# Kernel optimization log

Hardware: AMD Instinct MI355X
Metric: run time of the kernel (lower is better)

Reference implementation:

```python
import jax, jax.numpy as jnp
import numpy as np

NUM_TOKENS = 8192
CODEBOOK_DIM = 64
ENC_CH = 512
DEC_CH = 512
B, H, W = 16, 32, 32


def setup_inputs() -> dict:
    key = jax.random.key(0)
    ks = jax.random.split(key, 6)
    return {
        "x": jax.random.normal(ks[0], (B, ENC_CH, H, W), dtype=jnp.float32),
        "w_in": jax.random.normal(ks[1], (CODEBOOK_DIM, ENC_CH), dtype=jnp.float32) * 0.05,
        "b_in": jax.random.normal(ks[2], (CODEBOOK_DIM,), dtype=jnp.float32) * 0.05,
        "embedding": jax.random.normal(ks[3], (NUM_TOKENS, CODEBOOK_DIM), dtype=jnp.float32),
        "w_out": jax.random.normal(ks[4], (DEC_CH, CODEBOOK_DIM), dtype=jnp.float32) * 0.05,
        "b_out": jax.random.normal(ks[5], (DEC_CH,), dtype=jnp.float32) * 0.05,
    }


def reference(x, w_in, b_in, embedding, w_out, b_out):
    # encoder projection: 1x1 conv == channel matmul. x: [B,C,H,W] -> [B,d,H,W]
    z = jnp.einsum('bchw,dc->bdhw', x, w_in) + b_in[None, :, None, None]

    # VectorQuantizer.forward -----------------------------------------
    # permute to channels-last and flatten: [B,H,W,d] -> [N,d]
    inputs = jnp.transpose(z, (0, 2, 3, 1))  # [B,H,W,d]
    flat = inputs.reshape(-1, CODEBOOK_DIM)  # [N,d]

    # squared L2 distances to every codebook entry: [N,K]
    distances = (jnp.sum(flat ** 2, axis=1, keepdims=True)
                 + jnp.sum(embedding ** 2, axis=1)[None, :]
                 - 2.0 * flat @ embedding.T)
    indices = jnp.argmin(distances, axis=1)  # [N] int

    # one-hot @ embedding in the original == direct gather
    quantized = jnp.take(embedding, indices, axis=0).reshape(inputs.shape)

    # straight-through estimator
    quantized = inputs + jax.lax.stop_gradient(quantized - inputs)
    tokens = jnp.transpose(quantized, (0, 3, 1, 2))  # [B,d,H,W]

    # decoder projection: 1x1 conv
    projected = jnp.einsum('bdhw,od->bohw', tokens, w_out) + b_out[None, :, None, None]
    return projected, indices
```

## Files before the change

### kernel.cpp

```cpp
#include <hip/hip_runtime.h>

#define NROWS 16384
#define DDIM 64
#define KCB 8192
#define CIN 512
#define OUTC 512
#define OUT_MAIN 8388608

typedef float f4 __attribute__((ext_vector_type(4)));
typedef float f32x16 __attribute__((ext_vector_type(16)));
typedef __bf16 bf16x4 __attribute__((ext_vector_type(4)));
typedef __bf16 bf16x8 __attribute__((ext_vector_type(8)));

#define OFF_ZBF 0
#define OFF_EBF 1572864
#define OFF_E2H 2359296
#define OFF_PMV 2367488
#define OFF_PMI 2629632
#define ZS_STRIDE 1048576
#define ES_STRIDE 524288

__global__ __launch_bounds__(256) void k_enc(const float* __restrict__ x,
                                             const float* __restrict__ w_in,
                                             const float* __restrict__ b_in,
                                             __bf16* __restrict__ zbf) {
  __shared__ float Wt[128][36];
  const int bid = blockIdx.x;
  const int g = bid >> 1, dh = bid & 1;
  const int b = g >> 5, h = g & 31;
  const int d0 = dh * 32;
  const int t = threadIdx.x;
  const int w = t & 31, dg = t >> 5;
  float acc[4];
#pragma unroll
  for (int j = 0; j < 4; ++j) acc[j] = b_in[d0 + dg * 4 + j];
  const float* xb = x + ((size_t)b * CIN * 1024) + h * 32 + w;
  for (int c0 = 0; c0 < CIN; c0 += 128) {
    __syncthreads();
#pragma unroll
    for (int i = 0; i < 16; ++i) {
      int e = t + 256 * i;
      int cc = e & 127, dd = e >> 7;
      Wt[cc][dd] = w_in[(size_t)(d0 + dd) * CIN + c0 + cc];
    }
    __syncthreads();
#pragma unroll 8
    for (int c = 0; c < 128; ++c) {
      float xv = xb[(size_t)(c0 + c) * 1024];
      const f4 wv = *(const f4*)&Wt[c][dg * 4];
      acc[0] = fmaf(xv, wv.x, acc[0]);
      acc[1] = fmaf(xv, wv.y, acc[1]);
      acc[2] = fmaf(xv, wv.z, acc[2]);
      acc[3] = fmaf(xv, wv.w, acc[3]);
    }
  }
  const int K0 = dh * 32 + dg * 4;
  const int kb = K0 >> 4, khalf = (K0 >> 3) & 1, j0 = K0 & 7;
  bf16x4 s0, s1, s2;
#pragma unroll
  for (int j = 0; j < 4; ++j) {
    float v = acc[j];
    __bf16 a0 = (__bf16)v;
    float r1 = v - (float)a0;
    __bf16 a1 = (__bf16)r1;
    float r2 = r1 - (float)a1;
    __bf16 a2 = (__bf16)r2;
    s0[j] = a0; s1[j] = a1; s2[j] = a2;
  }
  const size_t base = ((size_t)(kb * 512 + g) * 64 + khalf * 32 + w) * 8 + j0;
  *(bf16x4*)(zbf + base) = s0;
  *(bf16x4*)(zbf + base + ZS_STRIDE) = s1;
  *(bf16x4*)(zbf + base + 2 * ZS_STRIDE) = s2;
}

__global__ __launch_bounds__(256) void k_prep(const float* __restrict__ emb,
                                              __bf16* __restrict__ ebf,
                                              float* __restrict__ e2h) {
  __shared__ float s2[4][64];
  const int C0 = blockIdx.x * 64;
  const int t = threadIdx.x;
  const int cl = t & 63, kb = t >> 6;
  const int c = C0 + cl;
  const int cg = blockIdx.x * 2 + (cl >> 5);
  float e[16];
  {
    const f4* ep = (const f4*)(emb + (size_t)c * DDIM + kb * 16);
#pragma unroll
    for (int q = 0; q < 4; ++q) {
      f4 v = ep[q];
      e[q * 4 + 0] = v.x; e[q * 4 + 1] = v.y; e[q * 4 + 2] = v.z; e[q * 4 + 3] = v.w;
    }
  }
  float sq = 0.f;
#pragma unroll
  for (int i = 0; i < 16; ++i) sq = fmaf(e[i], e[i], sq);
  s2[kb][cl] = sq;
  bf16x8 v0[2], v1[2], v2[2];
#pragma unroll
  for (int i = 0; i < 16; ++i) {
    float v = e[i];
    __bf16 a0 = (__bf16)v;
    float r1 = v - (float)a0;
    __bf16 a1 = (__bf16)r1;
    float r2 = r1 - (float)a1;
    __bf16 a2 = (__bf16)r2;
    v0[i >> 3][i & 7] = a0; v1[i >> 3][i & 7] = a1; v2[i >> 3][i & 7] = a2;
  }
#pragma unroll
  for (int khalf = 0; khalf < 2; ++khalf) {
    const size_t dst = ((size_t)(kb * 256 + cg) * 64 + khalf * 32 + (cl & 31)) * 8;
    *(bf16x8*)(ebf + dst) = v0[khalf];
    *(bf16x8*)(ebf + dst + ES_STRIDE) = v1[khalf];
    *(bf16x8*)(ebf + dst + 2 * ES_STRIDE) = v2[khalf];
  }
  __syncthreads();
  if (t < 64)
    e2h[C0 + t] = 0.5f * (s2[0][t] + s2[1][t] + s2[2][t] + s2[3][t]);
}

__global__ __launch_bounds__(256, 3) void k_argmin(const __bf16* __restrict__ zbf,
                                                   const __bf16* __restrict__ ebf,
                                                   const float* __restrict__ e2h,
                                                   float* __restrict__ pmv,
                                                   int* __restrict__ pmi) {
  __shared__ __bf16 Als[2][6144];
  const int bid = blockIdx.x;
  const int rowblk = bid >> 4, chunk = bid & 15;
  const int t = threadIdx.x;
  const int l = t & 63;
  const int wv = t >> 6;
  const int h4 = (l >> 5) * 4;
  const int g = rowblk * 4 + wv;

  bf16x8 zf[3][4];
#pragma unroll
  for (int s = 0; s < 3; ++s)
#pragma unroll
    for (int kb = 0; kb < 4; ++kb)
      zf[s][kb] = *(const bf16x8*)(zbf + (size_t)s * ZS_STRIDE +
                                   ((size_t)(kb * 512 + g) * 64 + l) * 8);

  float mv = -3.4028235e38f;
  int mi = 0;

  auto stage = [&](int st, int bi) {
    const int cg = chunk * 16 + st;
#pragma unroll
    for (int i = 0; i < 3; ++i) {
      const int fi = wv * 3 + i;
      const int s = fi >> 2, kb = fi & 3;
      const __bf16* src = ebf + (size_t)s * ES_STRIDE +
                          ((size_t)(kb * 256 + cg) * 64 + l) * 8;
      __builtin_amdgcn_global_load_lds(
          (const __attribute__((address_space(1))) void*)src,
          (__attribute__((address_space(3))) void*)&Als[bi][fi * 512 + l * 8],
          16, 0, 0);
    }
  };

  stage(0, 0);
#pragma unroll 1
  for (int st = 0; st < 16; ++st) {
    __syncthreads();
    if (st + 1 < 16) stage(st + 1, (st + 1) & 1);
    const __bf16* B = &Als[st & 1][0];
    const int cbase = (chunk * 16 + st) * 32;
    f32x16 acc = (f32x16)(0.0f);
    bf16x8 af[4];
#define LDAF(b)                                                              \
  {                                                                          \
    _Pragma("unroll") for (int kb = 0; kb < 4; ++kb) af[kb] =                \
        *(const bf16x8*)(B + ((b)*4 + kb) * 512 + l * 8);                    \
  }
#define SW(a)                                                                \
  {                                                                          \
    _Pragma("unroll") for (int kb = 0; kb < 4; ++kb) acc =                   \
        __builtin_amdgcn_mfma_f32_32x32x16_bf16(af[kb], zf[a][kb], acc, 0,   \
                                                0, 0);                       \
  }
    LDAF(0); SW(0); SW(1); SW(2);
    LDAF(1); SW(0); SW(1);
    LDAF(2); SW(0);
#undef LDAF
#undef SW
    const float* e2p = e2h + cbase + h4;
#pragma unroll
    for (int q = 0; q < 4; ++q) {
      const f4 e2q = *(const f4*)(e2p + q * 8);
#pragma unroll
      for (int i = 0; i < 4; ++i) {
        const float s = acc[q * 4 + i] - e2q[i];
        if (s > mv) { mv = s; mi = cbase + h4 + q * 8 + i; }
      }
    }
  }
  {
    float ov = __shfl_xor(mv, 32);
    int oi = __shfl_xor(mi, 32);
    if (ov > mv || (ov == mv && oi < mi)) { mv = ov; mi = oi; }
  }
  if (l < 32) {
    const int row = rowblk * 128 + wv * 32 + l;
    pmv[chunk * NROWS + row] = mv;
    pmi[chunk * NROWS + row] = mi;
  }
}

__global__ __launch_bounds__(256) void k_pick(const float* __restrict__ pmv,
                                              const int* __restrict__ pmi,
                                              float* __restrict__ idxf) {
  int n = blockIdx.x * 256 + threadIdx.x;
  float bv = pmv[n];
  int bi = pmi[n];
#pragma unroll
  for (int p = 1; p < 16; ++p) {
    float v = pmv[p * NROWS + n];
    int i = pmi[p * NROWS + n];
    if (v > bv) { bv = v; bi = i; }
  }
  idxf[n] = (float)bi;
}

__global__ __launch_bounds__(256) void k_dec(const float* __restrict__ emb,
                                             const float* __restrict__ w_out,
                                             const float* __restrict__ b_out,
                                             const float* __restrict__ idxf,
                                             float* __restrict__ out) {
  __shared__ float Qt[DDIM][36];
  __shared__ float Wt[DDIM][68];
  const int bid = blockIdx.x;
  const int bh = bid >> 1, oh = bid & 1;
  const int b = bh >> 5, h = bh & 31;
  const int t = threadIdx.x;
  const int w = t & 31, og = t >> 5;
  {
    const int dd = t & 63, r4 = t >> 6;
#pragma unroll
    for (int i = 0; i < 8; ++i) {
      int r = r4 + 4 * i;
      int qi = (int)idxf[bh * 32 + r];
      Qt[dd][r] = emb[(size_t)qi * DDIM + dd];
    }
  }
  for (int ob = 0; ob < 4; ++ob) {
    const int o0 = oh * 256 + ob * 64;
    __syncthreads();
#pragma unroll
    for (int i = 0; i < 16; ++i) {
      int e = t + 256 * i;
      int oo = e >> 6, dd = e & 63;
      Wt[dd][oo] = w_out[(size_t)(o0 + oo) * DDIM + dd];
    }
    __syncthreads();
    float a[8];
#pragma unroll
    for (int j = 0; j < 8; ++j) a[j] = b_out[o0 + og * 8 + j];
#pragma unroll 4
    for (int d = 0; d < 64; ++d) {
      float qv = Qt[d][w];
      const f4 w0 = *(const f4*)&Wt[d][og * 8];
      const f4 w1 = *(const f4*)&Wt[d][og * 8 + 4];
      a[0] = fmaf(qv, w0.x, a[0]);
      a[1] = fmaf(qv, w0.y, a[1]);
      a[2] = fmaf(qv, w0.z, a[2]);
      a[3] = fmaf(qv, w0.w, a[3]);
      a[4] = fmaf(qv, w1.x, a[4]);
      a[5] = fmaf(qv, w1.y, a[5]);
      a[6] = fmaf(qv, w1.z, a[6]);
      a[7] = fmaf(qv, w1.w, a[7]);
    }
    float* op = out + (((size_t)b * OUTC + o0 + og * 8) * 32 + h) * 32 + w;
#pragma unroll
    for (int j = 0; j < 8; ++j) op[(size_t)j * 1024] = a[j];
  }
}

extern "C" void kernel_launch(void* const* d_in, const int* in_sizes, int n_in,
                              void* d_out, int out_size, void* d_ws, size_t ws_size,
                              hipStream_t stream) {
  const float* x = (const float*)d_in[0];
  const float* w_in = (const float*)d_in[1];
  const float* b_in = (const float*)d_in[2];
  const float* emb = (const float*)d_in[3];
  const float* w_out = (const float*)d_in[4];
  const float* b_out = (const float*)d_in[5];
  float* out = (float*)d_out;

  __bf16* zbf = (__bf16*)(out + OFF_ZBF);
  __bf16* ebf = (__bf16*)(out + OFF_EBF);
  float* e2h = out + OFF_E2H;
  float* pmv = out + OFF_PMV;
  int* pmi = (int*)(out + OFF_PMI);
  float* idxf = out + OUT_MAIN;

  k_enc<<<1024, 256, 0, stream>>>(x, w_in, b_in, zbf);
  k_prep<<<128, 256, 0, stream>>>(emb, ebf, e2h);
  k_argmin<<<2048, 256, 0, stream>>>(zbf, ebf, e2h, pmv, pmi);
  k_pick<<<64, 256, 0, stream>>>(pmv, pmi, idxf);
  k_dec<<<1024, 256, 0, stream>>>(emb, w_out, b_out, idxf, out);
}
```

Measured before the change: 242.6 us.

## Rewrite encoder and decoder projections to wave-uniform scalar weight loads

The encoder and decoder 1x1-conv kernels drop their LDS staging and barriers. Each wavefront now owns a fixed slice of output channels, selected through readfirstlane, so weight reads are wave-uniform and can become scalar loads. Each lane owns one spatial position. In the decoder each lane holds its full quantized vector in registers, and the encoder writes bf16x8 splits. Grids shrink to 256 blocks of 512 threads, which lowers occupancy and uses fewer blocks than there are CUs, and register use rises.

```diff
diff --git a/kernel.cpp b/kernel.cpp
--- a/kernel.cpp
+++ b/kernel.cpp
@@ -20,57 +20,53 @@
 #define ZS_STRIDE 1048576
 #define ES_STRIDE 524288
 
-__global__ __launch_bounds__(256) void k_enc(const float* __restrict__ x,
+__global__ __launch_bounds__(512) void k_enc(const float* __restrict__ x,
                                              const float* __restrict__ w_in,
                                              const float* __restrict__ b_in,
                                              __bf16* __restrict__ zbf) {
-  __shared__ float Wt[128][36];
-  const int bid = blockIdx.x;
-  const int g = bid >> 1, dh = bid & 1;
-  const int b = g >> 5, h = g & 31;
-  const int d0 = dh * 32;
-  const int t = threadIdx.x;
-  const int w = t & 31, dg = t >> 5;
-  float acc[4];
-#pragma unroll
-  for (int j = 0; j < 4; ++j) acc[j] = b_in[d0 + dg * 4 + j];
-  const float* xb = x + ((size_t)b * CIN * 1024) + h * 32 + w;
-  for (int c0 = 0; c0 < CIN; c0 += 128) {
-    __syncthreads();
-#pragma unroll
-    for (int i = 0; i < 16; ++i) {
-      int e = t + 256 * i;
-      int cc = e & 127, dd = e >> 7;
-      Wt[cc][dd] = w_in[(size_t)(d0 + dd) * CIN + c0 + cc];
-    }
-    __syncthreads();
-#pragma unroll 8
-    for (int c = 0; c < 128; ++c) {
-      float xv = xb[(size_t)(c0 + c) * 1024];
-      const f4 wv = *(const f4*)&Wt[c][dg * 4];
-      acc[0] = fmaf(xv, wv.x, acc[0]);
-      acc[1] = fmaf(xv, wv.y, acc[1]);
-      acc[2] = fmaf(xv, wv.z, acc[2]);
-      acc[3] = fmaf(xv, wv.w, acc[3]);
-    }
-  }
-  const int K0 = dh * 32 + dg * 4;
-  const int kb = K0 >> 4, khalf = (K0 >> 3) & 1, j0 = K0 & 7;
-  bf16x4 s0, s1, s2;
-#pragma unroll
-  for (int j = 0; j < 4; ++j) {
+  const int t = threadIdx.x;
+  const int l = t & 63;
+  const int wv = __builtin_amdgcn_readfirstlane(t >> 6);
+  const int n = blockIdx.x * 64 + l;
+  const int b = n >> 10, hw = n & 1023;
+  const float* xp = x + ((size_t)b * CIN) * 1024 + hw;
+  const float* wrow = w_in + (size_t)(wv * 8) * CIN;
+
+  float acc[8];
+#pragma unroll
+  for (int j = 0; j < 8; ++j) acc[j] = 0.f;
+
+#pragma unroll 1
+  for (int c0 = 0; c0 < CIN; c0 += 16) {
+    float xv[16];
+#pragma unroll
+    for (int cc = 0; cc < 16; ++cc) xv[cc] = xp[(size_t)(c0 + cc) * 1024];
+#pragma unroll
+    for (int cc = 0; cc < 16; ++cc) {
+#pragma unroll
+      for (int j = 0; j < 8; ++j)
+        acc[j] = fmaf(xv[cc], wrow[j * CIN + c0 + cc], acc[j]);
+    }
+  }
+#pragma unroll
+  for (int j = 0; j < 8; ++j) acc[j] += b_in[wv * 8 + j];
+
+  const int kb = wv >> 1, khalf = wv & 1;
+  const int g = n >> 5, row = n & 31;
+  bf16x8 s0, s1, s2;
+#pragma unroll
+  for (int j = 0; j < 8; ++j) {
     float v = acc[j];
     __bf16 a0 = (__bf16)v;
     float r1 = v - (float)a0;
     __bf16 a1 = (__bf16)r1;
     float r2 = r1 - (float)a1;
-    __bf16 a2 = (__bf16)r2;
-    s0[j] = a0; s1[j] = a1; s2[j] = a2;
-  }
-  const size_t base = ((size_t)(kb * 512 + g) * 64 + khalf * 32 + w) * 8 + j0;
-  *(bf16x4*)(zbf + base) = s0;
-  *(bf16x4*)(zbf + base + ZS_STRIDE) = s1;
-  *(bf16x4*)(zbf + base + 2 * ZS_STRIDE) = s2;
+    s0[j] = a0; s1[j] = a1; s2[j] = (__bf16)r2;
+  }
+  const size_t base = ((size_t)(kb * 512 + g) * 64 + khalf * 32 + row) * 8;
+  *(bf16x8*)(zbf + base) = s0;
+  *(bf16x8*)(zbf + base + ZS_STRIDE) = s1;
+  *(bf16x8*)(zbf + base + 2 * ZS_STRIDE) = s2;
 }
 
 __global__ __launch_bounds__(256) void k_prep(const float* __restrict__ emb,
@@ -103,8 +99,7 @@
     float r1 = v - (float)a0;
     __bf16 a1 = (__bf16)r1;
     float r2 = r1 - (float)a1;
-    __bf16 a2 = (__bf16)r2;
-    v0[i >> 3][i & 7] = a0; v1[i >> 3][i & 7] = a1; v2[i >> 3][i & 7] = a2;
+    v0[i >> 3][i & 7] = a0; v1[i >> 3][i & 7] = a1; v2[i >> 3][i & 7] = (__bf16)r2;
   }
 #pragma unroll
   for (int khalf = 0; khalf < 2; ++khalf) {
@@ -221,57 +216,51 @@
   idxf[n] = (float)bi;
 }
 
-__global__ __launch_bounds__(256) void k_dec(const float* __restrict__ emb,
+__global__ __launch_bounds__(512) void k_dec(const float* __restrict__ emb,
                                              const float* __restrict__ w_out,
                                              const float* __restrict__ b_out,
                                              const float* __restrict__ idxf,
                                              float* __restrict__ out) {
-  __shared__ float Qt[DDIM][36];
-  __shared__ float Wt[DDIM][68];
-  const int bid = blockIdx.x;
-  const int bh = bid >> 1, oh = bid & 1;
-  const int b = bh >> 5, h = bh & 31;
-  const int t = threadIdx.x;
-  const int w = t & 31, og = t >> 5;
-  {
-    const int dd = t & 63, r4 = t >> 6;
-#pragma unroll
-    for (int i = 0; i < 8; ++i) {
-      int r = r4 + 4 * i;
-      int qi = (int)idxf[bh * 32 + r];
-      Qt[dd][r] = emb[(size_t)qi * DDIM + dd];
-    }
-  }
-  for (int ob = 0; ob < 4; ++ob) {
-    const int o0 = oh * 256 + ob * 64;
-    __syncthreads();
-#pragma unroll
-    for (int i = 0; i < 16; ++i) {
-      int e = t + 256 * i;
-      int oo = e >> 6, dd = e & 63;
-      Wt[dd][oo] = w_out[(size_t)(o0 + oo) * DDIM + dd];
-    }
-    __syncthreads();
-    float a[8];
-#pragma unroll
-    for (int j = 0; j < 8; ++j) a[j] = b_out[o0 + og * 8 + j];
-#pragma unroll 4
-    for (int d = 0; d < 64; ++d) {
-      float qv = Qt[d][w];
-      const f4 w0 = *(const f4*)&Wt[d][og * 8];
-      const f4 w1 = *(const f4*)&Wt[d][og * 8 + 4];
-      a[0] = fmaf(qv, w0.x, a[0]);
-      a[1] = fmaf(qv, w0.y, a[1]);
-      a[2] = fmaf(qv, w0.z, a[2]);
-      a[3] = fmaf(qv, w0.w, a[3]);
-      a[4] = fmaf(qv, w1.x, a[4]);
-      a[5] = fmaf(qv, w1.y, a[5]);
-      a[6] = fmaf(qv, w1.z, a[6]);
-      a[7] = fmaf(qv, w1.w, a[7]);
-    }
-    float* op = out + (((size_t)b * OUTC + o0 + og * 8) * 32 + h) * 32 + w;
-#pragma unroll
-    for (int j = 0; j < 8; ++j) op[(size_t)j * 1024] = a[j];
+  const int t = threadIdx.x;
+  const int l = t & 63;
+  const int wv = __builtin_amdgcn_readfirstlane(t >> 6);
+  const int n = blockIdx.x * 64 + l;
+  const int b = n >> 10, hw = n & 1023;
+  const int qi = (int)idxf[n];
+  const f4* qp = (const f4*)(emb + (size_t)qi * DDIM);
+  float* op = out + ((size_t)b * OUTC) * 1024 + hw;
+
+  f4 q[16];
+#pragma unroll
+  for (int i = 0; i < 16; ++i) q[i] = qp[i];
+
+#pragma unroll 1
+  for (int pass = 0; pass < 8; ++pass) {
+    const int o0 = wv * 64 + pass * 8;
+    const float* wr = w_out + (size_t)o0 * DDIM;
+    float acc[8];
+#pragma unroll
+    for (int jo = 0; jo < 8; ++jo) acc[jo] = b_out[o0 + jo];
+#pragma unroll
+    for (int dc = 0; dc < 8; ++dc) {
+      const f4 qa = q[dc * 2];
+      const f4 qb = q[dc * 2 + 1];
+#pragma unroll
+      for (int jo = 0; jo < 8; ++jo) {
+        const float* w8 = wr + jo * DDIM + dc * 8;
+        acc[jo] = fmaf(qa.x, w8[0], acc[jo]);
+        acc[jo] = fmaf(qa.y, w8[1], acc[jo]);
+        acc[jo] = fmaf(qa.z, w8[2], acc[jo]);
+        acc[jo] = fmaf(qa.w, w8[3], acc[jo]);
+        acc[jo] = fmaf(qb.x, w8[4], acc[jo]);
+        acc[jo] = fmaf(qb.y, w8[5], acc[jo]);
+        acc[jo] = fmaf(qb.z, w8[6], acc[jo]);
+        acc[jo] = fmaf(qb.w, w8[7], acc[jo]);
+      }
+    }
+#pragma unroll
+    for (int jo = 0; jo < 8; ++jo)
+      op[(size_t)(o0 + jo) * 1024] = acc[jo];
   }
 }
 
@@ -293,9 +282,9 @@
   int* pmi = (int*)(out + OFF_PMI);
   float* idxf = out + OUT_MAIN;
 
-  k_enc<<<1024, 256, 0, stream>>>(x, w_in, b_in, zbf);
+  k_enc<<<256, 512, 0, stream>>>(x, w_in, b_in, zbf);
   k_prep<<<128, 256, 0, stream>>>(emb, ebf, e2h);
   k_argmin<<<2048, 256, 0, stream>>>(zbf, ebf, e2h, pmv, pmi);
   k_pick<<<64, 256, 0, stream>>>(pmv, pmi, idxf);
-  k_dec<<<1024, 256, 0, stream>>>(emb, w_out, b_out, idxf, out);
-}
+  k_dec<<<256, 512, 0, stream>>>(emb, w_out, b_out, idxf, out);
+}
```

Result: slower. 279.8 us (+15.3%).
